# Kernel optimization log

Measured on AMD Instinct MI355X. Metric: run time of the kernel, lower is better.

The kernel has to match this reference:

```python
import jax, jax.numpy as jnp
import numpy as np

IN_FEATURES = 2048
OUT_FEATURES = 2048
BLOCK_SIZE = 16
F_BLOCKS = (OUT_FEATURES + BLOCK_SIZE - 1) // BLOCK_SIZE  # 128
G_BLOCKS = (IN_FEATURES + BLOCK_SIZE - 1) // BLOCK_SIZE   # 128
BATCH = 4096


def setup_inputs() -> dict:
    key = jax.random.key(0)
    k1, k2, k3 = jax.random.split(key, 3)
    x = jax.random.normal(k1, (BATCH, IN_FEATURES), dtype=jnp.float32)
    # Xavier-uniform-ish scale for index vectors viewed as (f*g, block_size)
    limit = np.sqrt(6.0 / (F_BLOCKS * G_BLOCKS + BLOCK_SIZE)).astype(np.float32)
    index_vectors = jax.random.uniform(
        k2, (F_BLOCKS, G_BLOCKS, BLOCK_SIZE), dtype=jnp.float32,
        minval=-limit, maxval=limit)
    b = jax.random.normal(k3, (OUT_FEATURES,), dtype=jnp.float32) * 0.02
    return {"x": x, "index_vectors": index_vectors, "b": b}


def reference(x, index_vectors, b):
    batch = x.shape[0]
    padded_in = G_BLOCKS * BLOCK_SIZE
    padded_out = F_BLOCKS * BLOCK_SIZE
    if x.shape[1] < padded_in:
        x = jnp.pad(x, ((0, 0), (0, padded_in - x.shape[1])))
    x_blocks = x.reshape(batch, G_BLOCKS, BLOCK_SIZE)            # (B, g, b)
    # Batched FFT over all blocks at once (replaces the f*g python loop)
    fft_p = jnp.fft.fft(index_vectors, axis=-1)                  # (f, g, b) complex
    fft_x = jnp.fft.fft(x_blocks, axis=-1)                       # (B, g, b) complex
    # sum_j IFFT(P_ij * X_j) == IFFT(sum_j P_ij * X_j) by linearity of IFFT
    out_fft = jnp.einsum('fgb,Bgb->Bfb', fft_p, fft_x)           # (B, f, b) complex
    out_blocks = jnp.fft.ifft(out_fft, axis=-1).real             # (B, f, b)
    out = out_blocks.reshape(batch, padded_out)
    if padded_out > OUT_FEATURES:
        out = out[:, :OUT_FEATURES]
    return out + b
```

## Files before the change

### kernel.cpp

```cpp
#include <hip/hip_runtime.h>
#include <hip/hip_bf16.h>


#define M_DIM 4096
#define N_DIM 2048
#define K_DIM 2048
#define BK 64
#define NT (K_DIM / BK)
#define BUFSZ 49152

typedef __attribute__((ext_vector_type(8))) short bf16x8;
typedef __attribute__((ext_vector_type(4))) float f32x4;

typedef const __attribute__((address_space(1))) void gvoid_t;
typedef __attribute__((address_space(3))) void lvoid_t;

#define FENCE asm volatile("" ::: "memory")
#define BAR()  do { FENCE; __builtin_amdgcn_s_barrier(); FENCE; } while (0)
#define GLD(src, dst) __builtin_amdgcn_global_load_lds((gvoid_t*)(src), (lvoid_t*)(dst), 16, 0, 0)

#define STAGE_A(dst, src) (GLD((src) + 0 * 64 * K_DIM, (dst) + 0),     \
                           GLD((src) + 1 * 64 * K_DIM, (dst) + 8192),  \
                           GLD((src) + 2 * 64 * K_DIM, (dst) + 16384), \
                           GLD((src) + 3 * 64 * K_DIM, (dst) + 24576))
#define STAGE_B(dst, src) (GLD((src) + 0 * 64 * K_DIM, (dst) + 0),     \
                           GLD((src) + 1 * 64 * K_DIM, (dst) + 8192))

__device__ __forceinline__ unsigned int f2bf(float f) {
  unsigned int u = __float_as_uint(f);
  return (u + 0x7fffu + ((u >> 16) & 1u)) >> 16;
}

__global__ __launch_bounds__(256) void prep_kernel(const float* __restrict__ x,
                                                   const float* __restrict__ iv,
                                                   unsigned short* __restrict__ xb,
                                                   unsigned short* __restrict__ W) {
  int b = blockIdx.x;
  if (b < (M_DIM * K_DIM / 8) / 256) {
    int idx = b * 256 + threadIdx.x;
    const float4* x4 = (const float4*)x;
    float4 a = x4[idx * 2 + 0];
    float4 c = x4[idx * 2 + 1];
    uint4 o;
    o.x = f2bf(a.x) | (f2bf(a.y) << 16);
    o.y = f2bf(a.z) | (f2bf(a.w) << 16);
    o.z = f2bf(c.x) | (f2bf(c.y) << 16);
    o.w = f2bf(c.z) | (f2bf(c.w) << 16);
    ((uint4*)xb)[idx] = o;
  } else {
    int idx = (b - (M_DIM * K_DIM / 8) / 256) * 256 + threadIdx.x;
    int o  = idx >> 8;
    int i0 = (idx & 255) * 8;
    int f = o >> 4, t = o & 15;
    int g = i0 >> 4, u0 = i0 & 15;
    const float* row = iv + (f * 128 + g) * 16;
    unsigned int p[4];
#pragma unroll
    for (int j = 0; j < 4; ++j) {
      unsigned int lo = f2bf(row[(t - (u0 + 2 * j + 0)) & 15]);
      unsigned int hi = f2bf(row[(t - (u0 + 2 * j + 1)) & 15]);
      p[j] = lo | (hi << 16);
    }
    ((uint4*)W)[idx] = make_uint4(p[0], p[1], p[2], p[3]);
  }
}

__global__ __launch_bounds__(512, 2) void gemm_bias_kernel(const unsigned short* __restrict__ A,
                                                           const unsigned short* __restrict__ B,
                                                           const float* __restrict__ bias,
                                                           float* __restrict__ C) {
  __shared__ char lds[3 * BUFSZ];

  const int tid = threadIdx.x;
  const int l   = tid & 63;
  const int w   = tid >> 6;
  const int wm  = w >> 1;
  const int wn  = w & 1;

  const int orig = blockIdx.x;
  const int swz  = (orig & 7) * 32 + (orig >> 3);
  const int bm   = swz >> 4;
  const int bn   = swz & 15;

  f32x4 acc[4][4] = {};

  const int srow  = w * 8 + (l >> 3);
  const int sslot = (l & 7) ^ ((l >> 3) & 7);
  const unsigned short* Asrc0 = A + (size_t)(bm * 256 + srow) * K_DIM + sslot * 8;
  const unsigned short* Bsrc0 = B + (size_t)(bn * 128 + srow) * K_DIM + sslot * 8;

  const int fr = l & 15;
  const int rxor = (l & 7) << 4;
  const int aRow0 = (wm * 64 + fr) * 128;
  const int bRow0 = (wn * 64 + fr) * 128;
  const int swzcol0 = (0 * 64 + (l >> 4) * 16) ^ rxor;
  const int swzcol1 = (1 * 64 + (l >> 4) * 16) ^ rxor;

#define PHASE(Ab, Bb, SWZ, STAGE_STMT)                                  \
  do {                                                                  \
    bf16x8 a_[4], b_[4];                                                \
    _Pragma("unroll")                                                   \
    for (int m = 0; m < 4; ++m)                                         \
      a_[m] = *(const bf16x8*)((Ab) + aRow0 + m * 2048 + (SWZ));        \
    _Pragma("unroll")                                                   \
    for (int n = 0; n < 4; ++n)                                         \
      b_[n] = *(const bf16x8*)((Bb) + bRow0 + n * 2048 + (SWZ));        \
    STAGE_STMT;                                                         \
    BAR();                                                              \
    asm volatile("s_waitcnt lgkmcnt(0)" ::: "memory");                  \
    __builtin_amdgcn_sched_barrier(0);                                  \
    __builtin_amdgcn_s_setprio(1);                                      \
    _Pragma("unroll")                                                   \
    for (int m = 0; m < 4; ++m)                                         \
      _Pragma("unroll")                                                 \
      for (int n = 0; n < 4; ++n)                                       \
        acc[m][n] = __builtin_amdgcn_mfma_f32_16x16x32_bf16(a_[m], b_[n], acc[m][n], 0, 0, 0); \
    __builtin_amdgcn_s_setprio(0);                                      \
    __builtin_amdgcn_sched_barrier(0);                                  \
    BAR();                                                              \
  } while (0)

#define TILE_T(t_, CUR_, NB_)                                           \
  do {                                                                  \
    const char* Ab = lds + (CUR_) * BUFSZ;                              \
    const char* Bb = Ab + 32768;                                        \
    char* Ad = lds + (NB_) * BUFSZ + w * 1024;                          \
    char* Bd = lds + (NB_) * BUFSZ + 32768 + w * 1024;                  \
    const unsigned short* as2 = Asrc0 + ((t_) + 2) * BK;                \
    const unsigned short* bs2 = Bsrc0 + ((t_) + 2) * BK;                \
    PHASE(Ab, Bb, swzcol0, STAGE_A(Ad, as2));                           \
    PHASE(Ab, Bb, swzcol1, STAGE_B(Bd, bs2));                           \
    asm volatile("s_waitcnt vmcnt(6)" ::: "memory");                    \
    BAR();                                                              \
  } while (0)

  STAGE_A(lds + 0 * BUFSZ + w * 1024, Asrc0 + 0 * BK);
  STAGE_B(lds + 0 * BUFSZ + 32768 + w * 1024, Bsrc0 + 0 * BK);
  STAGE_A(lds + 1 * BUFSZ + w * 1024, Asrc0 + 1 * BK);
  STAGE_B(lds + 1 * BUFSZ + 32768 + w * 1024, Bsrc0 + 1 * BK);
  asm volatile("s_waitcnt vmcnt(6)" ::: "memory");
  BAR();

  for (int t = 0; t < NT - 2; t += 3) {
    TILE_T(t + 0, 0, 2);
    TILE_T(t + 1, 1, 0);
    TILE_T(t + 2, 2, 1);
  }

  {
    const char* Ab = lds + 0 * BUFSZ;
    const char* Bb = Ab + 32768;
    PHASE(Ab, Bb, swzcol0, (void)0);
    PHASE(Ab, Bb, swzcol1, (void)0);
    asm volatile("s_waitcnt vmcnt(0)" ::: "memory");
    BAR();
  }
  {
    const char* Ab = lds + 1 * BUFSZ;
    const char* Bb = Ab + 32768;
    PHASE(Ab, Bb, swzcol0, (void)0);
    PHASE(Ab, Bb, swzcol1, (void)0);
  }

  const int row0 = bm * 256 + wm * 64 + (l >> 4) * 4;
  const int col0 = bn * 128 + wn * 64 + (l & 15);
#pragma unroll
  for (int n = 0; n < 4; ++n) {
    float bv = bias[col0 + n * 16];
#pragma unroll
    for (int m = 0; m < 4; ++m) {
#pragma unroll
      for (int j = 0; j < 4; ++j) {
        C[(size_t)(row0 + m * 16 + j) * N_DIM + (col0 + n * 16)] = acc[m][n][j] + bv;
      }
    }
  }
#undef TILE_T
#undef PHASE
}

__global__ __launch_bounds__(256) void fallback_kernel(const float* __restrict__ x,
                                                       const float* __restrict__ iv,
                                                       const float* __restrict__ b,
                                                       float* __restrict__ out) {
  int idx = blockIdx.x * 256 + threadIdx.x;
  int Bn = idx >> 11, o = idx & 2047;
  int f = o >> 4, t = o & 15;
  const float* xr = x + (size_t)Bn * 2048;
  float acc = 0.f;
  for (int g = 0; g < 128; ++g) {
    const float* pr = iv + (f * 128 + g) * 16;
    const float* xg = xr + g * 16;
#pragma unroll
    for (int s = 0; s < 16; ++s) acc += pr[s] * xg[(t - s) & 15];
  }
  out[idx] = acc + b[o];
}

extern "C" void kernel_launch(void* const* d_in, const int* in_sizes, int n_in,
                              void* d_out, int out_size, void* d_ws, size_t ws_size,
                              hipStream_t stream) {
  const float* x    = (const float*)d_in[0];
  const float* iv   = (const float*)d_in[1];
  const float* bias = (const float*)d_in[2];
  float* out = (float*)d_out;

  const size_t xb_bytes = (size_t)M_DIM * K_DIM * 2;
  const size_t w_bytes  = (size_t)N_DIM * K_DIM * 2;
  if (ws_size < xb_bytes + w_bytes) {
    fallback_kernel<<<(M_DIM * N_DIM) / 256, 256, 0, stream>>>(x, iv, bias, out);
    return;
  }

  unsigned short* xb = (unsigned short*)d_ws;
  unsigned short* W  = xb + (size_t)M_DIM * K_DIM;

  const int cvt_blocks = (M_DIM * K_DIM / 8) / 256;
  const int bw_blocks  = (N_DIM * K_DIM / 8) / 256;
  prep_kernel<<<cvt_blocks + bw_blocks, 256, 0, stream>>>(x, iv, xb, W);

  gemm_bias_kernel<<<(M_DIM / 256) * (N_DIM / 128), 512, 0, stream>>>(xb, W, bias, out);
}
```

Measured before the change: 57.21 us.

## Double-buffer LDS fragment registers to overlap ds_reads with MFMA

Restructures the GEMM main loop so each K-subtile's LDS fragment loads are issued into a second register set while MFMAs run on the previously loaded fragments. Partial lgkmcnt waits replace the full drain, and the number of barriers per tile drops from five to two. The aim is to hide LDS read latency behind matrix math. The cost is higher VGPR pressure from the extra fragment registers, and the changed vmcnt and barrier placement carries a risk of races on the triple-buffered LDS.

```diff
diff --git a/kernel.cpp b/kernel.cpp
--- a/kernel.cpp
+++ b/kernel.cpp
@@ -96,41 +96,44 @@
   const int swzcol0 = (0 * 64 + (l >> 4) * 16) ^ rxor;
   const int swzcol1 = (1 * 64 + (l >> 4) * 16) ^ rxor;
 
-#define PHASE(Ab, Bb, SWZ, STAGE_STMT)                                  \
+  bf16x8 fa0[4], fb0[4], fa1[4], fb1[4];
+
+#define LDA(SA, SB, BUF, SWZ)                                           \
   do {                                                                  \
-    bf16x8 a_[4], b_[4];                                                \
+    const char* Ab_ = lds + (BUF) * BUFSZ;                              \
+    const char* Bb_ = Ab_ + 32768;                                      \
     _Pragma("unroll")                                                   \
     for (int m = 0; m < 4; ++m)                                         \
-      a_[m] = *(const bf16x8*)((Ab) + aRow0 + m * 2048 + (SWZ));        \
+      SA[m] = *(const bf16x8*)(Ab_ + aRow0 + m * 2048 + (SWZ));         \
     _Pragma("unroll")                                                   \
     for (int n = 0; n < 4; ++n)                                         \
-      b_[n] = *(const bf16x8*)((Bb) + bRow0 + n * 2048 + (SWZ));        \
-    STAGE_STMT;                                                         \
-    BAR();                                                              \
-    asm volatile("s_waitcnt lgkmcnt(0)" ::: "memory");                  \
+      SB[n] = *(const bf16x8*)(Bb_ + bRow0 + n * 2048 + (SWZ));         \
+  } while (0)
+
+#define MM(SA, SB, CNT)                                                 \
+  do {                                                                  \
+    asm volatile("s_waitcnt lgkmcnt(" #CNT ")" ::: "memory");           \
     __builtin_amdgcn_sched_barrier(0);                                  \
     __builtin_amdgcn_s_setprio(1);                                      \
     _Pragma("unroll")                                                   \
     for (int m = 0; m < 4; ++m)                                         \
       _Pragma("unroll")                                                 \
       for (int n = 0; n < 4; ++n)                                       \
-        acc[m][n] = __builtin_amdgcn_mfma_f32_16x16x32_bf16(a_[m], b_[n], acc[m][n], 0, 0, 0); \
+        acc[m][n] = __builtin_amdgcn_mfma_f32_16x16x32_bf16(SA[m], SB[n], acc[m][n], 0, 0, 0); \
     __builtin_amdgcn_s_setprio(0);                                      \
     __builtin_amdgcn_sched_barrier(0);                                  \
+  } while (0)
+
+#define TILE_FULL(CUR, NXT, STG, T)                                     \
+  do {                                                                  \
+    LDA(fa1, fb1, CUR, swzcol1);                                        \
+    STAGE_A(lds + (STG) * BUFSZ + w * 1024, Asrc0 + ((T) + 2) * BK);    \
+    MM(fa0, fb0, 8);                                                    \
+    asm volatile("s_waitcnt vmcnt(4)" ::: "memory");                    \
     BAR();                                                              \
-  } while (0)
-
-#define TILE_T(t_, CUR_, NB_)                                           \
-  do {                                                                  \
-    const char* Ab = lds + (CUR_) * BUFSZ;                              \
-    const char* Bb = Ab + 32768;                                        \
-    char* Ad = lds + (NB_) * BUFSZ + w * 1024;                          \
-    char* Bd = lds + (NB_) * BUFSZ + 32768 + w * 1024;                  \
-    const unsigned short* as2 = Asrc0 + ((t_) + 2) * BK;                \
-    const unsigned short* bs2 = Bsrc0 + ((t_) + 2) * BK;                \
-    PHASE(Ab, Bb, swzcol0, STAGE_A(Ad, as2));                           \
-    PHASE(Ab, Bb, swzcol1, STAGE_B(Bd, bs2));                           \
-    asm volatile("s_waitcnt vmcnt(6)" ::: "memory");                    \
+    LDA(fa0, fb0, NXT, swzcol0);                                        \
+    STAGE_B(lds + (STG) * BUFSZ + 32768 + w * 1024, Bsrc0 + ((T) + 2) * BK); \
+    MM(fa1, fb1, 8);                                                    \
     BAR();                                                              \
   } while (0)
 
@@ -140,27 +143,23 @@
   STAGE_B(lds + 1 * BUFSZ + 32768 + w * 1024, Bsrc0 + 1 * BK);
   asm volatile("s_waitcnt vmcnt(6)" ::: "memory");
   BAR();
+  LDA(fa0, fb0, 0, swzcol0);
 
   for (int t = 0; t < NT - 2; t += 3) {
-    TILE_T(t + 0, 0, 2);
-    TILE_T(t + 1, 1, 0);
-    TILE_T(t + 2, 2, 1);
-  }
-
-  {
-    const char* Ab = lds + 0 * BUFSZ;
-    const char* Bb = Ab + 32768;
-    PHASE(Ab, Bb, swzcol0, (void)0);
-    PHASE(Ab, Bb, swzcol1, (void)0);
-    asm volatile("s_waitcnt vmcnt(0)" ::: "memory");
-    BAR();
-  }
-  {
-    const char* Ab = lds + 1 * BUFSZ;
-    const char* Bb = Ab + 32768;
-    PHASE(Ab, Bb, swzcol0, (void)0);
-    PHASE(Ab, Bb, swzcol1, (void)0);
-  }
+    TILE_FULL(0, 1, 2, t);
+    TILE_FULL(1, 2, 0, t + 1);
+    TILE_FULL(2, 0, 1, t + 2);
+  }
+
+  LDA(fa1, fb1, 0, swzcol1);
+  MM(fa0, fb0, 8);
+  asm volatile("s_waitcnt vmcnt(0)" ::: "memory");
+  BAR();
+  LDA(fa0, fb0, 1, swzcol0);
+  MM(fa1, fb1, 8);
+  LDA(fa1, fb1, 1, swzcol1);
+  MM(fa0, fb0, 8);
+  MM(fa1, fb1, 0);
 
   const int row0 = bm * 256 + wm * 64 + (l >> 4) * 4;
   const int col0 = bn * 128 + wn * 64 + (l & 15);
@@ -175,8 +174,9 @@
       }
     }
   }
-#undef TILE_T
-#undef PHASE
+#undef TILE_FULL
+#undef MM
+#undef LDA
 }
 
 __global__ __launch_bounds__(256) void fallback_kernel(const float* __restrict__ x,
```

Result: faster. 55.10 us (-3.7%).
